# Optimization experiments

Measured on AMD Instinct MI355X. Metric: run time of the kernel, lower is better.

## Reference

```python
import jax, jax.numpy as jnp
import numpy as np

B, N, S, D, H = 32, 16384, 8, 64, 128  # batch, num_inputs, num_slots, slot_size(==input_size), mlp_hidden
ITERS = 3
EPS = 1e-8
LN_EPS = 1e-5


def _ln(x, g, b):
    m = jnp.mean(x, axis=-1, keepdims=True)
    v = jnp.mean((x - m) ** 2, axis=-1, keepdims=True)
    return (x - m) * jax.lax.rsqrt(v + LN_EPS) * g + b


def setup_inputs() -> dict:
    key = jax.random.key(0)
    ks = jax.random.split(key, 20)
    s = 0.02
    return {
        "x": jax.random.normal(ks[0], (B, N, D), jnp.float32),
        "slot_noise": jax.random.normal(ks[1], (B, S, D), jnp.float32),
        "slots_mu": jax.random.normal(ks[2], (1, S, D), jnp.float32),
        "slots_log_sigma": jax.random.normal(ks[3], (1, S, D), jnp.float32) * 0.1,
        "ln_in_g": jnp.ones((D,), jnp.float32), "ln_in_b": jnp.zeros((D,), jnp.float32),
        "ln_slot_g": jnp.ones((D,), jnp.float32), "ln_slot_b": jnp.zeros((D,), jnp.float32),
        "ln_mlp_g": jnp.ones((D,), jnp.float32), "ln_mlp_b": jnp.zeros((D,), jnp.float32),
        "Wq": jax.random.normal(ks[4], (D, D), jnp.float32) * s,
        "Wk": jax.random.normal(ks[5], (D, D), jnp.float32) * s,
        "Wv": jax.random.normal(ks[6], (D, D), jnp.float32) * s,
        "W_ih": jax.random.normal(ks[7], (3 * D, D), jnp.float32) * s,
        "W_hh": jax.random.normal(ks[8], (3 * D, D), jnp.float32) * s,
        "b_ih": jnp.zeros((3 * D,), jnp.float32),
        "b_hh": jnp.zeros((3 * D,), jnp.float32),
        "W1": jax.random.normal(ks[9], (H, D), jnp.float32) * s,
        "b1": jnp.zeros((H,), jnp.float32),
        "W2": jax.random.normal(ks[10], (D, H), jnp.float32) * s,
        "b2": jnp.zeros((D,), jnp.float32),
    }


def reference(x, slot_noise, slots_mu, slots_log_sigma,
              ln_in_g, ln_in_b, ln_slot_g, ln_slot_b, ln_mlp_g, ln_mlp_b,
              Wq, Wk, Wv, W_ih, W_hh, b_ih, b_hh, W1, b1, W2, b2):
    inputs = _ln(x, ln_in_g, ln_in_b)                      # [B,N,D]
    keys = inputs @ Wk.T                                   # [B,N,D]
    values = inputs @ Wv.T                                 # [B,N,D]
    slots = slots_mu + jnp.exp(slots_log_sigma) * slot_noise  # [B,S,D]
    scale = D ** (-0.5)
    for _ in range(ITERS):
        slots_prev = slots
        q = (_ln(slots, ln_slot_g, ln_slot_b) @ Wq.T) * scale   # [B,S,D]
        attn = jax.nn.softmax(jnp.einsum('bnd,bsd->bns', keys, q), axis=2) + EPS
        attn = attn / jnp.sum(attn, axis=1, keepdims=True)      # weighted mean over inputs
        updates = jnp.einsum('bns,bnd->bsd', attn, values)      # [B,S,D]
        # GRUCell(update, hidden=slots_prev), torch semantics
        gi = updates @ W_ih.T + b_ih
        gh = slots_prev @ W_hh.T + b_hh
        i_r, i_z, i_n = jnp.split(gi, 3, axis=-1)
        h_r, h_z, h_n = jnp.split(gh, 3, axis=-1)
        r = jax.nn.sigmoid(i_r + h_r)
        z = jax.nn.sigmoid(i_z + h_z)
        n = jnp.tanh(i_n + r * h_n)
        upd = (1.0 - z) * n + z * slots_prev
        # residual MLP (full_skip=False: residual around updates)
        slots = upd + jax.nn.relu(_ln(upd, ln_mlp_g, ln_mlp_b) @ W1.T + b1) @ W2.T + b2
    return slots
```

## Files before the change

kernel.cpp:

```cpp
#include <hip/hip_runtime.h>

#define BB 32
#define NN 16384

typedef __attribute__((ext_vector_type(4))) float f4;
typedef __attribute__((ext_vector_type(8))) short short8;

__device__ __forceinline__ unsigned int f2bf(float f) {
  unsigned int u = __float_as_uint(f);
  return (u + 0x7fffu + ((u >> 16) & 1u)) >> 16;
}
__device__ __forceinline__ short bfs(float f) { return (short)f2bf(f); }

__global__ void __launch_bounds__(256) prep_kernel(
    const float* __restrict__ Wk, const float* __restrict__ Wv,
    unsigned short* __restrict__ Wkb, unsigned short* __restrict__ Wvb)
{
  int id = blockIdx.x * 256 + threadIdx.x;
  Wkb[id] = (unsigned short)f2bf(Wk[id]);
  Wvb[id] = (unsigned short)f2bf(Wv[id]);
}

__global__ void __launch_bounds__(64) init_q_kernel(
    const float* __restrict__ noise, const float* __restrict__ mu,
    const float* __restrict__ lsig, float* __restrict__ slots,
    const float* __restrict__ gs, const float* __restrict__ bsl,
    const float* __restrict__ Wq, unsigned short* __restrict__ qb)
{
  const int bsi = blockIdx.x, l = threadIdx.x;
  const int idx = bsi * 64 + l;
  __shared__ float sh[64];
  float v = mu[idx & 511] + __expf(lsig[idx & 511]) * noise[idx];
  slots[idx] = v;
  float sm = v, sq = v * v;
#pragma unroll
  for (int m = 1; m < 64; m <<= 1) { sm += __shfl_xor(sm, m); sq += __shfl_xor(sq, m); }
  float mean = sm * (1.f / 64.f);
  float var = sq * (1.f / 64.f) - mean * mean;
  sh[l] = (v - mean) * rsqrtf(var + 1e-5f) * gs[l] + bsl[l];
  float acc = 0.f;
  const float* w = Wq + l * 64;
  for (int k = 0; k < 64; ++k) acc += sh[k] * w[k];
  qb[idx] = (unsigned short)f2bf(acc * 0.125f);
}

__global__ void __launch_bounds__(256) proj_kernel(
    const float* __restrict__ x, const float* __restrict__ gin, const float* __restrict__ bin,
    const unsigned short* __restrict__ Wkb, const unsigned short* __restrict__ Wvb,
    unsigned short* __restrict__ Kf, unsigned short* __restrict__ Vtf)
{
  const int blk = blockIdx.x;
  const int tid = threadIdx.x, wave = tid >> 6, lane = tid & 63;
  const int l15 = lane & 15, quad = lane >> 4;
  const int b = blk >> 6;
  const size_t row0 = ((size_t)blk << 8) + (wave << 4) + l15;
  const float* xp = x + row0 * 64 + quad * 8;

  const int k0 = quad * 8;
  f4 g0a = *(const f4*)(gin + k0),      g0b = *(const f4*)(gin + k0 + 4);
  f4 g1a = *(const f4*)(gin + k0 + 32), g1b = *(const f4*)(gin + k0 + 36);
  f4 h0a = *(const f4*)(bin + k0),      h0b = *(const f4*)(bin + k0 + 4);
  f4 h1a = *(const f4*)(bin + k0 + 32), h1b = *(const f4*)(bin + k0 + 36);

  f4 c0 = *(const f4*)xp, c1 = *(const f4*)(xp + 4);
  f4 c2 = *(const f4*)(xp + 32), c3 = *(const f4*)(xp + 36);

  for (int g = 0; g < 4; ++g) {
    f4 p0, p1, p2, p3;
    if (g < 3) {
      const float* np = xp + (size_t)(g + 1) * 4096;
      p0 = *(const f4*)np;        p1 = *(const f4*)(np + 4);
      p2 = *(const f4*)(np + 32); p3 = *(const f4*)(np + 36);
    }
    float sm = 0.f, sq = 0.f;
#pragma unroll
    for (int j = 0; j < 4; ++j) {
      float v0 = c0[j], v1 = c1[j], v2 = c2[j], v3 = c3[j];
      sm += v0 + v1 + v2 + v3;
      sq += v0 * v0 + v1 * v1 + v2 * v2 + v3 * v3;
    }
    sm += __shfl_xor(sm, 16); sq += __shfl_xor(sq, 16);
    sm += __shfl_xor(sm, 32); sq += __shfl_xor(sq, 32);
    const float mean = sm * (1.f / 64.f);
    const float var = sq * (1.f / 64.f) - mean * mean;
    const float rstd = rsqrtf(var + 1e-5f);

    short8 a0, a1;
#pragma unroll
    for (int j = 0; j < 4; ++j) {
      a0[j]     = bfs((c0[j] - mean) * rstd * g0a[j] + h0a[j]);
      a0[j + 4] = bfs((c1[j] - mean) * rstd * g0b[j] + h0b[j]);
      a1[j]     = bfs((c2[j] - mean) * rstd * g1a[j] + h1a[j]);
      a1[j + 4] = bfs((c3[j] - mean) * rstd * g1b[j] + h1b[j]);
    }

    const int nblk = ((blk & 63) << 4) + (g << 2) + wave;
    unsigned short* kbase = Kf + (((size_t)b << 20) + (nblk << 10));
    unsigned short* vbase = Vtf + (((size_t)b << 20) + (nblk << 10));

#pragma unroll
    for (int dt = 0; dt < 4; ++dt) {
      const unsigned short* wkp = Wkb + ((dt << 4) + l15) * 64 + k0;
      const unsigned short* wvp = Wvb + ((dt << 4) + l15) * 64 + k0;
      short8 wk0 = *(const short8*)wkp, wk1 = *(const short8*)(wkp + 32);
      short8 wv0 = *(const short8*)wvp, wv1 = *(const short8*)(wvp + 32);
      f4 ak = {0.f, 0.f, 0.f, 0.f}, av = {0.f, 0.f, 0.f, 0.f};
      ak = __builtin_amdgcn_mfma_f32_16x16x32_bf16(wk0, a0, ak, 0, 0, 0);
      ak = __builtin_amdgcn_mfma_f32_16x16x32_bf16(wk1, a1, ak, 0, 0, 0);
      av = __builtin_amdgcn_mfma_f32_16x16x32_bf16(a0, wv0, av, 0, 0, 0);
      av = __builtin_amdgcn_mfma_f32_16x16x32_bf16(a1, wv1, av, 0, 0, 0);
      uint2 kk;
      kk.x = f2bf(ak[0]) | (f2bf(ak[1]) << 16);
      kk.y = f2bf(ak[2]) | (f2bf(ak[3]) << 16);
      *(uint2*)(kbase + (((dt << 1) + (quad >> 1)) << 7) + (l15 << 3) + ((quad & 1) << 2)) = kk;
      uint2 vv;
      vv.x = f2bf(av[0]) | (f2bf(av[1]) << 16);
      vv.y = f2bf(av[2]) | (f2bf(av[3]) << 16);
      *(uint2*)(vbase + (((dt << 4) + l15) << 4) + (quad << 2)) = vv;
    }
    c0 = p0; c1 = p1; c2 = p2; c3 = p3;
  }
}

__global__ void __launch_bounds__(256) reduce_kernel(
    const unsigned short* __restrict__ Kf, const unsigned short* __restrict__ Vtf,
    const unsigned short* __restrict__ qb,
    float* __restrict__ Wpart, float* __restrict__ cpart)
{
  __shared__ __align__(16) unsigned short Pt[4][16][40];
  __shared__ float red[4][512];
  __shared__ float cred[4][8];

  const int tid = threadIdx.x, wave = tid >> 6, lane = tid & 63;
  const int l15 = lane & 15, quad = lane >> 4;
  const int b = blockIdx.x >> 6, ch = blockIdx.x & 63;

  const unsigned short* qrow = qb + (((b << 3) + (l15 & 7)) << 6) + quad * 8;
  short8 qf0 = *(const short8*)qrow;
  short8 qf1 = *(const short8*)(qrow + 32);

  const unsigned short* Kb = Kf + ((size_t)b << 20);
  const unsigned short* Vb = Vtf + ((size_t)b << 20);

  f4 wacc[4];
#pragma unroll
  for (int t = 0; t < 4; ++t) wacc[t] = (f4){0.f, 0.f, 0.f, 0.f};
  float cacc = 0.f;
  const int nb0 = (ch << 8) + (wave << 6);

#pragma unroll
  for (int u = 0; u < 2; ++u) {
    const int nb = nb0 + u * 32;
    const int nblk0 = nb >> 4;
    const unsigned short* ka = Kb + (nblk0 << 10) + (quad << 7) + (l15 << 3);
    short8 ka0 = *(const short8*)ka;
    short8 ka1 = *(const short8*)(ka + 512);
    short8 kb0 = *(const short8*)(ka + 1024);
    short8 kb1 = *(const short8*)(ka + 1536);
    short8 vf[4];
#pragma unroll
    for (int t = 0; t < 4; ++t)
      vf[t] = *(const short8*)(Vb + ((nblk0 + (quad >> 1)) << 10) +
                               (((t << 4) + l15) << 4) + ((quad & 1) << 3));

#pragma unroll
    for (int h = 0; h < 2; ++h) {
      f4 lg = {0.f, 0.f, 0.f, 0.f};
      lg = __builtin_amdgcn_mfma_f32_16x16x32_bf16(h ? kb0 : ka0, qf0, lg, 0, 0, 0);
      lg = __builtin_amdgcn_mfma_f32_16x16x32_bf16(h ? kb1 : ka1, qf1, lg, 0, 0, 0);
      float p[4];
#pragma unroll
      for (int r2 = 0; r2 < 4; ++r2) {
        float e = __expf(lg[r2]);
        float ss = e;
        ss += __shfl_xor(ss, 1);
        ss += __shfl_xor(ss, 2);
        ss += __shfl_xor(ss, 4);
        p[r2] = e * __builtin_amdgcn_rcpf(ss);
        cacc += p[r2];
      }
      unsigned short* pw = &Pt[wave][l15][h * 16 + quad * 4];
      *(unsigned int*)pw = f2bf(p[0]) | (f2bf(p[1]) << 16);
      *(unsigned int*)(pw + 2) = f2bf(p[2]) | (f2bf(p[3]) << 16);
    }
    short8 pf = *(const short8*)&Pt[wave][l15][quad * 8];
#pragma unroll
    for (int t = 0; t < 4; ++t)
      wacc[t] = __builtin_amdgcn_mfma_f32_16x16x32_bf16(pf, vf[t], wacc[t], 0, 0, 0);
  }

  cacc += __shfl_xor(cacc, 16);
  cacc += __shfl_xor(cacc, 32);
  if (lane < 8) cred[wave][lane] = cacc;
  if (quad < 2) {
#pragma unroll
    for (int t = 0; t < 4; ++t)
#pragma unroll
      for (int r2 = 0; r2 < 4; ++r2)
        red[wave][(quad * 4 + r2) * 64 + (t << 4) + l15] = wacc[t][r2];
  }
  __syncthreads();
  for (int i = tid; i < 512; i += 256)
    Wpart[(size_t)blockIdx.x * 512 + i] = red[0][i] + red[1][i] + red[2][i] + red[3][i];
  if (tid < 8)
    cpart[blockIdx.x * 8 + tid] = cred[0][tid] + cred[1][tid] + cred[2][tid] + cred[3][tid];
}

__global__ void __launch_bounds__(256) update_kernel(
    const float* __restrict__ Wpart, const float* __restrict__ cpart,
    const float* __restrict__ slots, float* __restrict__ out,
    const float* __restrict__ W_ih, const float* __restrict__ W_hh,
    const float* __restrict__ b_ih, const float* __restrict__ b_hh,
    const float* __restrict__ g_mlp, const float* __restrict__ b_mlp,
    const float* __restrict__ W1, const float* __restrict__ b1,
    const float* __restrict__ W2, const float* __restrict__ b2,
    const float* __restrict__ gs, const float* __restrict__ bsl,
    const float* __restrict__ Wq, unsigned short* __restrict__ qb, int make_q)
{
  const int bs = blockIdx.x;
  const int b = bs >> 3, s = bs & 7;
  const int tid = threadIdx.x;
  const int l = tid & 63, cq = tid >> 6;
  __shared__ float wred[4][64];
  __shared__ float credS[4];
  __shared__ float u_sh[64], sp_sh[64], giA[192], ghA[192], uln_sh[64], h_sh[128];

  float wp = 0.f, cp2 = 0.f;
  for (int c = cq * 16; c < cq * 16 + 16; ++c) {
    wp += Wpart[(size_t)(((b << 6) + c) * 8 + s) * 64 + l];
    cp2 += cpart[((b << 6) + c) * 8 + s];
  }
  wred[cq][l] = wp;
  if (l == 0) credS[cq] = cp2;
  __syncthreads();

  float sp = 0.f;
  if (tid < 64) {
    const float cs = credS[0] + credS[1] + credS[2] + credS[3];
    const float u = (wred[0][l] + wred[1][l] + wred[2][l] + wred[3][l]) / cs;
    sp = slots[(b * 8 + s) * 64 + l];
    u_sh[l] = u; sp_sh[l] = sp;
  }
  __syncthreads();

  if (tid < 192) {
    float accI = b_ih[tid], accH = b_hh[tid];
    const float* wi = W_ih + tid * 64;
    const float* wh = W_hh + tid * 64;
    for (int k = 0; k < 64; ++k) { accI += u_sh[k] * wi[k]; accH += sp_sh[k] * wh[k]; }
    giA[tid] = accI; ghA[tid] = accH;
  }
  __syncthreads();

  float upd = 0.f;
  if (tid < 64) {
    const float rg = 1.f / (1.f + __expf(-(giA[l] + ghA[l])));
    const float zg = 1.f / (1.f + __expf(-(giA[64 + l] + ghA[64 + l])));
    const float ng = tanhf(giA[128 + l] + rg * ghA[128 + l]);
    upd = (1.f - zg) * ng + zg * sp;
    float sm = upd, sq = upd * upd;
#pragma unroll
    for (int m = 1; m < 64; m <<= 1) { sm += __shfl_xor(sm, m); sq += __shfl_xor(sq, m); }
    const float mean = sm * (1.f / 64.f);
    const float var = sq * (1.f / 64.f) - mean * mean;
    uln_sh[l] = (upd - mean) * rsqrtf(var + 1e-5f) * g_mlp[l] + b_mlp[l];
  }
  __syncthreads();

  if (tid < 128) {
    float acc = b1[tid];
    const float* w1 = W1 + tid * 64;
    for (int k = 0; k < 64; ++k) acc += uln_sh[k] * w1[k];
    h_sh[tid] = fmaxf(acc, 0.f);
  }
  __syncthreads();

  if (tid < 64) {
    float acc = b2[l];
    const float* w2 = W2 + l * 128;
    for (int k = 0; k < 128; ++k) acc += h_sh[k] * w2[k];
    const float sv = upd + acc;
    out[(b * 8 + s) * 64 + l] = sv;
    if (make_q) {
      float sm2 = sv, sq2 = sv * sv;
#pragma unroll
      for (int m = 1; m < 64; m <<= 1) { sm2 += __shfl_xor(sm2, m); sq2 += __shfl_xor(sq2, m); }
      const float mean2 = sm2 * (1.f / 64.f);
      const float var2 = sq2 * (1.f / 64.f) - mean2 * mean2;
      u_sh[l] = (sv - mean2) * rsqrtf(var2 + 1e-5f) * gs[l] + bsl[l];
      float qa = 0.f;
      const float* w = Wq + l * 64;
      for (int k = 0; k < 64; ++k) qa += u_sh[k] * w[k];
      qb[(b * 8 + s) * 64 + l] = (unsigned short)f2bf(qa * 0.125f);
    }
  }
}

extern "C" void kernel_launch(void* const* d_in, const int* in_sizes, int n_in,
                              void* d_out, int out_size, void* d_ws, size_t ws_size,
                              hipStream_t stream) {
  const float* x       = (const float*)d_in[0];
  const float* noise   = (const float*)d_in[1];
  const float* mu      = (const float*)d_in[2];
  const float* lsig    = (const float*)d_in[3];
  const float* ln_in_g = (const float*)d_in[4];
  const float* ln_in_b = (const float*)d_in[5];
  const float* ln_sl_g = (const float*)d_in[6];
  const float* ln_sl_b = (const float*)d_in[7];
  const float* ln_ml_g = (const float*)d_in[8];
  const float* ln_ml_b = (const float*)d_in[9];
  const float* Wq      = (const float*)d_in[10];
  const float* Wk      = (const float*)d_in[11];
  const float* Wv      = (const float*)d_in[12];
  const float* W_ih    = (const float*)d_in[13];
  const float* W_hh    = (const float*)d_in[14];
  const float* b_ih    = (const float*)d_in[15];
  const float* b_hh    = (const float*)d_in[16];
  const float* W1      = (const float*)d_in[17];
  const float* b1      = (const float*)d_in[18];
  const float* W2      = (const float*)d_in[19];
  const float* b2      = (const float*)d_in[20];

  unsigned short* Kw  = (unsigned short*)d_ws;
  unsigned short* Vt  = Kw + (size_t)BB * NN * 64;
  unsigned short* Wkb = Vt + (size_t)BB * NN * 64;
  unsigned short* Wvb = Wkb + 4096;
  unsigned short* qb  = Wvb + 4096;
  float* slots = (float*)(qb + 16384);
  float* Wpart = slots + 32 * 8 * 64;
  float* cpart = Wpart + (size_t)2048 * 512;

  prep_kernel<<<dim3(16), dim3(256), 0, stream>>>(Wk, Wv, Wkb, Wvb);
  init_q_kernel<<<dim3(256), dim3(64), 0, stream>>>(
      noise, mu, lsig, slots, ln_sl_g, ln_sl_b, Wq, qb);
  proj_kernel<<<dim3(2048), dim3(256), 0, stream>>>(
      x, ln_in_g, ln_in_b, Wkb, Wvb, Kw, Vt);

  for (int it = 0; it < 3; ++it) {
    reduce_kernel<<<dim3(2048), dim3(256), 0, stream>>>(Kw, Vt, qb, Wpart, cpart);
    update_kernel<<<dim3(256), dim3(256), 0, stream>>>(
        Wpart, cpart, slots, (it == 2) ? (float*)d_out : slots,
        W_ih, W_hh, b_ih, b_hh, ln_ml_g, ln_ml_b, W1, b1, W2, b2,
        ln_sl_g, ln_sl_b, Wq, qb, (it < 2) ? 1 : 0);
  }
}
```

Measured before the change: 350.7 us.

## Restructure K layout and softmax mapping; hoist x loads and reuse weight fragments

The projection kernel now loads and normalizes all four row groups first, then loops over output tiles with each weight fragment reused across the four groups. K is written in a new interleaved layout. In the reduce kernel the MFMA operand order is swapped so slots land on rows, which shortens the softmax reduction to one cross-lane shuffle. Probabilities are written transposed into LDS as single 16-bit stores. The column-sum accumulation now reads the bf16-rounded probabilities from LDS, which changes rounding slightly. Scalar LDS stores may cause bank conflicts, and holding more live registers may lower occupancy.

```diff
diff --git a/kernel.cpp b/kernel.cpp
--- a/kernel.cpp
+++ b/kernel.cpp
@@ -11,6 +11,9 @@
   return (u + 0x7fffu + ((u >> 16) & 1u)) >> 16;
 }
 __device__ __forceinline__ short bfs(float f) { return (short)f2bf(f); }
+__device__ __forceinline__ float bf2f(unsigned short h) {
+  return __uint_as_float(((unsigned int)h) << 16);
+}
 
 __global__ void __launch_bounds__(256) prep_kernel(
     const float* __restrict__ Wk, const float* __restrict__ Wv,
@@ -47,7 +50,7 @@
 __global__ void __launch_bounds__(256) proj_kernel(
     const float* __restrict__ x, const float* __restrict__ gin, const float* __restrict__ bin,
     const unsigned short* __restrict__ Wkb, const unsigned short* __restrict__ Wvb,
-    unsigned short* __restrict__ Kf, unsigned short* __restrict__ Vtf)
+    unsigned short* __restrict__ Ktb, unsigned short* __restrict__ Vtf)
 {
   const int blk = blockIdx.x;
   const int tid = threadIdx.x, wave = tid >> 6, lane = tid & 63;
@@ -55,75 +58,73 @@
   const int b = blk >> 6;
   const size_t row0 = ((size_t)blk << 8) + (wave << 4) + l15;
   const float* xp = x + row0 * 64 + quad * 8;
-
   const int k0 = quad * 8;
+
   f4 g0a = *(const f4*)(gin + k0),      g0b = *(const f4*)(gin + k0 + 4);
   f4 g1a = *(const f4*)(gin + k0 + 32), g1b = *(const f4*)(gin + k0 + 36);
   f4 h0a = *(const f4*)(bin + k0),      h0b = *(const f4*)(bin + k0 + 4);
   f4 h1a = *(const f4*)(bin + k0 + 32), h1b = *(const f4*)(bin + k0 + 36);
 
-  f4 c0 = *(const f4*)xp, c1 = *(const f4*)(xp + 4);
-  f4 c2 = *(const f4*)(xp + 32), c3 = *(const f4*)(xp + 36);
-
+  short8 a0[4], a1[4];
+#pragma unroll
   for (int g = 0; g < 4; ++g) {
-    f4 p0, p1, p2, p3;
-    if (g < 3) {
-      const float* np = xp + (size_t)(g + 1) * 4096;
-      p0 = *(const f4*)np;        p1 = *(const f4*)(np + 4);
-      p2 = *(const f4*)(np + 32); p3 = *(const f4*)(np + 36);
-    }
+    const float* p = xp + (size_t)g * 4096;
+    f4 c0 = *(const f4*)p,        c1 = *(const f4*)(p + 4);
+    f4 c2 = *(const f4*)(p + 32), c3 = *(const f4*)(p + 36);
     float sm = 0.f, sq = 0.f;
 #pragma unroll
     for (int j = 0; j < 4; ++j) {
-      float v0 = c0[j], v1 = c1[j], v2 = c2[j], v3 = c3[j];
-      sm += v0 + v1 + v2 + v3;
-      sq += v0 * v0 + v1 * v1 + v2 * v2 + v3 * v3;
+      sm += c0[j] + c1[j] + c2[j] + c3[j];
+      sq += c0[j]*c0[j] + c1[j]*c1[j] + c2[j]*c2[j] + c3[j]*c3[j];
     }
     sm += __shfl_xor(sm, 16); sq += __shfl_xor(sq, 16);
     sm += __shfl_xor(sm, 32); sq += __shfl_xor(sq, 32);
     const float mean = sm * (1.f / 64.f);
     const float var = sq * (1.f / 64.f) - mean * mean;
     const float rstd = rsqrtf(var + 1e-5f);
-
-    short8 a0, a1;
 #pragma unroll
     for (int j = 0; j < 4; ++j) {
-      a0[j]     = bfs((c0[j] - mean) * rstd * g0a[j] + h0a[j]);
-      a0[j + 4] = bfs((c1[j] - mean) * rstd * g0b[j] + h0b[j]);
-      a1[j]     = bfs((c2[j] - mean) * rstd * g1a[j] + h1a[j]);
-      a1[j + 4] = bfs((c3[j] - mean) * rstd * g1b[j] + h1b[j]);
-    }
-
-    const int nblk = ((blk & 63) << 4) + (g << 2) + wave;
-    unsigned short* kbase = Kf + (((size_t)b << 20) + (nblk << 10));
-    unsigned short* vbase = Vtf + (((size_t)b << 20) + (nblk << 10));
-
-#pragma unroll
-    for (int dt = 0; dt < 4; ++dt) {
-      const unsigned short* wkp = Wkb + ((dt << 4) + l15) * 64 + k0;
-      const unsigned short* wvp = Wvb + ((dt << 4) + l15) * 64 + k0;
-      short8 wk0 = *(const short8*)wkp, wk1 = *(const short8*)(wkp + 32);
-      short8 wv0 = *(const short8*)wvp, wv1 = *(const short8*)(wvp + 32);
+      a0[g][j]     = bfs((c0[j] - mean) * rstd * g0a[j] + h0a[j]);
+      a0[g][j + 4] = bfs((c1[j] - mean) * rstd * g0b[j] + h0b[j]);
+      a1[g][j]     = bfs((c2[j] - mean) * rstd * g1a[j] + h1a[j]);
+      a1[g][j + 4] = bfs((c3[j] - mean) * rstd * g1b[j] + h1b[j]);
+    }
+  }
+
+  const int nblk0 = ((blk & 63) << 4) + wave;
+  unsigned short* Kbase = Ktb + ((size_t)b << 20);
+  unsigned short* Vbase = Vtf + ((size_t)b << 20);
+
+#pragma unroll
+  for (int dt = 0; dt < 4; ++dt) {
+    const unsigned short* wkp = Wkb + ((dt << 4) + l15) * 64 + k0;
+    const unsigned short* wvp = Wvb + ((dt << 4) + l15) * 64 + k0;
+    short8 wk0 = *(const short8*)wkp, wk1 = *(const short8*)(wkp + 32);
+    short8 wv0 = *(const short8*)wvp, wv1 = *(const short8*)(wvp + 32);
+    const int koff = ((dt >> 1) << 9) + (l15 << 5) +
+                     ((((dt & 1) << 1) | (quad >> 1)) << 3) + ((quad & 1) << 2);
+    const int voff = (((dt << 4) + l15) << 4) + (quad << 2);
+#pragma unroll
+    for (int g = 0; g < 4; ++g) {
       f4 ak = {0.f, 0.f, 0.f, 0.f}, av = {0.f, 0.f, 0.f, 0.f};
-      ak = __builtin_amdgcn_mfma_f32_16x16x32_bf16(wk0, a0, ak, 0, 0, 0);
-      ak = __builtin_amdgcn_mfma_f32_16x16x32_bf16(wk1, a1, ak, 0, 0, 0);
-      av = __builtin_amdgcn_mfma_f32_16x16x32_bf16(a0, wv0, av, 0, 0, 0);
-      av = __builtin_amdgcn_mfma_f32_16x16x32_bf16(a1, wv1, av, 0, 0, 0);
-      uint2 kk;
+      ak = __builtin_amdgcn_mfma_f32_16x16x32_bf16(wk0, a0[g], ak, 0, 0, 0);
+      ak = __builtin_amdgcn_mfma_f32_16x16x32_bf16(wk1, a1[g], ak, 0, 0, 0);
+      av = __builtin_amdgcn_mfma_f32_16x16x32_bf16(a0[g], wv0, av, 0, 0, 0);
+      av = __builtin_amdgcn_mfma_f32_16x16x32_bf16(a1[g], wv1, av, 0, 0, 0);
+      const size_t nb10 = (size_t)(nblk0 + (g << 2)) << 10;
+      uint2 kk, vv;
       kk.x = f2bf(ak[0]) | (f2bf(ak[1]) << 16);
       kk.y = f2bf(ak[2]) | (f2bf(ak[3]) << 16);
-      *(uint2*)(kbase + (((dt << 1) + (quad >> 1)) << 7) + (l15 << 3) + ((quad & 1) << 2)) = kk;
-      uint2 vv;
       vv.x = f2bf(av[0]) | (f2bf(av[1]) << 16);
       vv.y = f2bf(av[2]) | (f2bf(av[3]) << 16);
-      *(uint2*)(vbase + (((dt << 4) + l15) << 4) + (quad << 2)) = vv;
-    }
-    c0 = p0; c1 = p1; c2 = p2; c3 = p3;
+      *(uint2*)(Kbase + nb10 + koff) = kk;
+      *(uint2*)(Vbase + nb10 + voff) = vv;
+    }
   }
 }
 
 __global__ void __launch_bounds__(256) reduce_kernel(
-    const unsigned short* __restrict__ Kf, const unsigned short* __restrict__ Vtf,
+    const unsigned short* __restrict__ Ktb, const unsigned short* __restrict__ Vtf,
     const unsigned short* __restrict__ qb,
     float* __restrict__ Wpart, float* __restrict__ cpart)
 {
@@ -139,7 +140,7 @@
   short8 qf0 = *(const short8*)qrow;
   short8 qf1 = *(const short8*)(qrow + 32);
 
-  const unsigned short* Kb = Kf + ((size_t)b << 20);
+  const unsigned short* Kb = Ktb + ((size_t)b << 20);
   const unsigned short* Vb = Vtf + ((size_t)b << 20);
 
   f4 wacc[4];
@@ -150,40 +151,37 @@
 
 #pragma unroll
   for (int u = 0; u < 2; ++u) {
-    const int nb = nb0 + u * 32;
-    const int nblk0 = nb >> 4;
-    const unsigned short* ka = Kb + (nblk0 << 10) + (quad << 7) + (l15 << 3);
-    short8 ka0 = *(const short8*)ka;
-    short8 ka1 = *(const short8*)(ka + 512);
-    short8 kb0 = *(const short8*)(ka + 1024);
-    short8 kb1 = *(const short8*)(ka + 1536);
+    const int nblk0 = (nb0 + u * 32) >> 4;
+    const unsigned short* kp = Kb + (nblk0 << 10) + (l15 << 5) + (quad << 3);
+    short8 k00 = *(const short8*)kp;
+    short8 k01 = *(const short8*)(kp + 512);
+    short8 k10 = *(const short8*)(kp + 1024);
+    short8 k11 = *(const short8*)(kp + 1536);
     short8 vf[4];
 #pragma unroll
     for (int t = 0; t < 4; ++t)
-      vf[t] = *(const short8*)(Vb + ((nblk0 + (quad >> 1)) << 10) +
+      vf[t] = *(const short8*)(Vb + ((size_t)(nblk0 + (quad >> 1)) << 10) +
                                (((t << 4) + l15) << 4) + ((quad & 1) << 3));
 
 #pragma unroll
-    for (int h = 0; h < 2; ++h) {
+    for (int nt = 0; nt < 2; ++nt) {
       f4 lg = {0.f, 0.f, 0.f, 0.f};
-      lg = __builtin_amdgcn_mfma_f32_16x16x32_bf16(h ? kb0 : ka0, qf0, lg, 0, 0, 0);
-      lg = __builtin_amdgcn_mfma_f32_16x16x32_bf16(h ? kb1 : ka1, qf1, lg, 0, 0, 0);
-      float p[4];
-#pragma unroll
-      for (int r2 = 0; r2 < 4; ++r2) {
-        float e = __expf(lg[r2]);
-        float ss = e;
-        ss += __shfl_xor(ss, 1);
-        ss += __shfl_xor(ss, 2);
-        ss += __shfl_xor(ss, 4);
-        p[r2] = e * __builtin_amdgcn_rcpf(ss);
-        cacc += p[r2];
-      }
-      unsigned short* pw = &Pt[wave][l15][h * 16 + quad * 4];
-      *(unsigned int*)pw = f2bf(p[0]) | (f2bf(p[1]) << 16);
-      *(unsigned int*)(pw + 2) = f2bf(p[2]) | (f2bf(p[3]) << 16);
+      lg = __builtin_amdgcn_mfma_f32_16x16x32_bf16(qf0, nt ? k10 : k00, lg, 0, 0, 0);
+      lg = __builtin_amdgcn_mfma_f32_16x16x32_bf16(qf1, nt ? k11 : k01, lg, 0, 0, 0);
+      float e0 = __expf(lg[0]), e1 = __expf(lg[1]);
+      float e2 = __expf(lg[2]), e3 = __expf(lg[3]);
+      float ss = (e0 + e1) + (e2 + e3);
+      ss += __shfl_xor(ss, 16);
+      const float inv = __builtin_amdgcn_rcpf(ss);
+      const int col = nt * 16 + l15;
+      Pt[wave][quad * 4 + 0][col] = (unsigned short)f2bf(e0 * inv);
+      Pt[wave][quad * 4 + 1][col] = (unsigned short)f2bf(e1 * inv);
+      Pt[wave][quad * 4 + 2][col] = (unsigned short)f2bf(e2 * inv);
+      Pt[wave][quad * 4 + 3][col] = (unsigned short)f2bf(e3 * inv);
     }
     short8 pf = *(const short8*)&Pt[wave][l15][quad * 8];
+#pragma unroll
+    for (int i = 0; i < 8; ++i) cacc += bf2f((unsigned short)pf[i]);
 #pragma unroll
     for (int t = 0; t < 4; ++t)
       wacc[t] = __builtin_amdgcn_mfma_f32_16x16x32_bf16(pf, vf[t], wacc[t], 0, 0, 0);
@@ -321,8 +319,8 @@
   const float* W2      = (const float*)d_in[19];
   const float* b2      = (const float*)d_in[20];
 
-  unsigned short* Kw  = (unsigned short*)d_ws;
-  unsigned short* Vt  = Kw + (size_t)BB * NN * 64;
+  unsigned short* Ktb = (unsigned short*)d_ws;
+  unsigned short* Vt  = Ktb + (size_t)BB * NN * 64;
   unsigned short* Wkb = Vt + (size_t)BB * NN * 64;
   unsigned short* Wvb = Wkb + 4096;
   unsigned short* qb  = Wvb + 4096;
@@ -334,10 +332,10 @@
   init_q_kernel<<<dim3(256), dim3(64), 0, stream>>>(
       noise, mu, lsig, slots, ln_sl_g, ln_sl_b, Wq, qb);
   proj_kernel<<<dim3(2048), dim3(256), 0, stream>>>(
-      x, ln_in_g, ln_in_b, Wkb, Wvb, Kw, Vt);
+      x, ln_in_g, ln_in_b, Wkb, Wvb, Ktb, Vt);
 
   for (int it = 0; it < 3; ++it) {
-    reduce_kernel<<<dim3(2048), dim3(256), 0, stream>>>(Kw, Vt, qb, Wpart, cpart);
+    reduce_kernel<<<dim3(2048), dim3(256), 0, stream>>>(Ktb, Vt, qb, Wpart, cpart);
     update_kernel<<<dim3(256), dim3(256), 0, stream>>>(
         Wpart, cpart, slots, (it == 2) ? (float*)d_out : slots,
         W_ih, W_hh, b_ih, b_hh, ln_ml_g, ln_ml_b, W1, b1, W2, b2,
```

After: 361.7 us. +3.1%, slower.

## Halve proj/reduce grids and software-pipeline K/V loads in reduce kernel

Applied to the files above, without the earlier changes.

Proj and reduce kernels now each handle 512 rows per block instead of 256, so each grid shrinks from 2048 to 1024 blocks. The reduce kernel gains a register double-buffered loop that prefetches the next 32-row K/V tile while the current tile's logits, softmax and value accumulation run. This aims to hide global load latency and cut the partial-sum traffic and work in the update kernel. The cost is more registers per thread and fewer blocks to spread across the GPU's compute units.

```diff
diff --git a/kernel.cpp b/kernel.cpp
--- a/kernel.cpp
+++ b/kernel.cpp
@@ -52,8 +52,8 @@
   const int blk = blockIdx.x;
   const int tid = threadIdx.x, wave = tid >> 6, lane = tid & 63;
   const int l15 = lane & 15, quad = lane >> 4;
-  const int b = blk >> 6;
-  const size_t row0 = ((size_t)blk << 8) + (wave << 4) + l15;
+  const int b = blk >> 5;
+  const size_t row0 = ((size_t)blk << 9) + (wave << 4) + l15;
   const float* xp = x + row0 * 64 + quad * 8;
 
   const int k0 = quad * 8;
@@ -65,9 +65,9 @@
   f4 c0 = *(const f4*)xp, c1 = *(const f4*)(xp + 4);
   f4 c2 = *(const f4*)(xp + 32), c3 = *(const f4*)(xp + 36);
 
-  for (int g = 0; g < 4; ++g) {
+  for (int g = 0; g < 8; ++g) {
     f4 p0, p1, p2, p3;
-    if (g < 3) {
+    if (g < 7) {
       const float* np = xp + (size_t)(g + 1) * 4096;
       p0 = *(const f4*)np;        p1 = *(const f4*)(np + 4);
       p2 = *(const f4*)(np + 32); p3 = *(const f4*)(np + 36);
@@ -94,7 +94,7 @@
       a1[j + 4] = bfs((c3[j] - mean) * rstd * g1b[j] + h1b[j]);
     }
 
-    const int nblk = ((blk & 63) << 4) + (g << 2) + wave;
+    const int nblk = ((blk & 31) << 5) + (g << 2) + wave;
     unsigned short* kbase = Kf + (((size_t)b << 20) + (nblk << 10));
     unsigned short* vbase = Vtf + (((size_t)b << 20) + (nblk << 10));
 
@@ -133,7 +133,7 @@
 
   const int tid = threadIdx.x, wave = tid >> 6, lane = tid & 63;
   const int l15 = lane & 15, quad = lane >> 4;
-  const int b = blockIdx.x >> 6, ch = blockIdx.x & 63;
+  const int b = blockIdx.x >> 5, ch = blockIdx.x & 31;
 
   const unsigned short* qrow = qb + (((b << 3) + (l15 & 7)) << 6) + quad * 8;
   short8 qf0 = *(const short8*)qrow;
@@ -146,28 +146,42 @@
 #pragma unroll
   for (int t = 0; t < 4; ++t) wacc[t] = (f4){0.f, 0.f, 0.f, 0.f};
   float cacc = 0.f;
-  const int nb0 = (ch << 8) + (wave << 6);
-
-#pragma unroll
-  for (int u = 0; u < 2; ++u) {
-    const int nb = nb0 + u * 32;
-    const int nblk0 = nb >> 4;
-    const unsigned short* ka = Kb + (nblk0 << 10) + (quad << 7) + (l15 << 3);
-    short8 ka0 = *(const short8*)ka;
-    short8 ka1 = *(const short8*)(ka + 512);
-    short8 kb0 = *(const short8*)(ka + 1024);
-    short8 kb1 = *(const short8*)(ka + 1536);
-    short8 vf[4];
+  const int nblk_base = (ch << 5) + (wave << 3);
+
+  short8 ck[4], cv[4];
+  {
+    const unsigned short* ka = Kb + (nblk_base << 10) + (quad << 7) + (l15 << 3);
+    ck[0] = *(const short8*)ka;
+    ck[1] = *(const short8*)(ka + 512);
+    ck[2] = *(const short8*)(ka + 1024);
+    ck[3] = *(const short8*)(ka + 1536);
 #pragma unroll
     for (int t = 0; t < 4; ++t)
-      vf[t] = *(const short8*)(Vb + ((nblk0 + (quad >> 1)) << 10) +
+      cv[t] = *(const short8*)(Vb + ((size_t)(nblk_base + (quad >> 1)) << 10) +
                                (((t << 4) + l15) << 4) + ((quad & 1) << 3));
+  }
+
+#pragma unroll
+  for (int u = 0; u < 4; ++u) {
+    short8 nk[4], nv[4];
+    if (u < 3) {
+      const int nblk = nblk_base + 2 * (u + 1);
+      const unsigned short* ka = Kb + (nblk << 10) + (quad << 7) + (l15 << 3);
+      nk[0] = *(const short8*)ka;
+      nk[1] = *(const short8*)(ka + 512);
+      nk[2] = *(const short8*)(ka + 1024);
+      nk[3] = *(const short8*)(ka + 1536);
+#pragma unroll
+      for (int t = 0; t < 4; ++t)
+        nv[t] = *(const short8*)(Vb + ((size_t)(nblk + (quad >> 1)) << 10) +
+                                 (((t << 4) + l15) << 4) + ((quad & 1) << 3));
+    }
 
 #pragma unroll
     for (int h = 0; h < 2; ++h) {
       f4 lg = {0.f, 0.f, 0.f, 0.f};
-      lg = __builtin_amdgcn_mfma_f32_16x16x32_bf16(h ? kb0 : ka0, qf0, lg, 0, 0, 0);
-      lg = __builtin_amdgcn_mfma_f32_16x16x32_bf16(h ? kb1 : ka1, qf1, lg, 0, 0, 0);
+      lg = __builtin_amdgcn_mfma_f32_16x16x32_bf16(ck[h * 2], qf0, lg, 0, 0, 0);
+      lg = __builtin_amdgcn_mfma_f32_16x16x32_bf16(ck[h * 2 + 1], qf1, lg, 0, 0, 0);
       float p[4];
 #pragma unroll
       for (int r2 = 0; r2 < 4; ++r2) {
@@ -186,7 +200,10 @@
     short8 pf = *(const short8*)&Pt[wave][l15][quad * 8];
 #pragma unroll
     for (int t = 0; t < 4; ++t)
-      wacc[t] = __builtin_amdgcn_mfma_f32_16x16x32_bf16(pf, vf[t], wacc[t], 0, 0, 0);
+      wacc[t] = __builtin_amdgcn_mfma_f32_16x16x32_bf16(pf, cv[t], wacc[t], 0, 0, 0);
+
+#pragma unroll
+    for (int i = 0; i < 4; ++i) { ck[i] = nk[i]; cv[i] = nv[i]; }
   }
 
   cacc += __shfl_xor(cacc, 16);
@@ -226,9 +243,9 @@
   __shared__ float u_sh[64], sp_sh[64], giA[192], ghA[192], uln_sh[64], h_sh[128];
 
   float wp = 0.f, cp2 = 0.f;
-  for (int c = cq * 16; c < cq * 16 + 16; ++c) {
-    wp += Wpart[(size_t)(((b << 6) + c) * 8 + s) * 64 + l];
-    cp2 += cpart[((b << 6) + c) * 8 + s];
+  for (int c = cq * 8; c < cq * 8 + 8; ++c) {
+    wp += Wpart[(size_t)(((b << 5) + c) * 8 + s) * 64 + l];
+    cp2 += cpart[((b << 5) + c) * 8 + s];
   }
   wred[cq][l] = wp;
   if (l == 0) credS[cq] = cp2;
@@ -328,16 +345,16 @@
   unsigned short* qb  = Wvb + 4096;
   float* slots = (float*)(qb + 16384);
   float* Wpart = slots + 32 * 8 * 64;
-  float* cpart = Wpart + (size_t)2048 * 512;
+  float* cpart = Wpart + (size_t)1024 * 512;
 
   prep_kernel<<<dim3(16), dim3(256), 0, stream>>>(Wk, Wv, Wkb, Wvb);
   init_q_kernel<<<dim3(256), dim3(64), 0, stream>>>(
       noise, mu, lsig, slots, ln_sl_g, ln_sl_b, Wq, qb);
-  proj_kernel<<<dim3(2048), dim3(256), 0, stream>>>(
+  proj_kernel<<<dim3(1024), dim3(256), 0, stream>>>(
       x, ln_in_g, ln_in_b, Wkb, Wvb, Kw, Vt);
 
   for (int it = 0; it < 3; ++it) {
-    reduce_kernel<<<dim3(2048), dim3(256), 0, stream>>>(Kw, Vt, qb, Wpart, cpart);
+    reduce_kernel<<<dim3(1024), dim3(256), 0, stream>>>(Kw, Vt, qb, Wpart, cpart);
     update_kernel<<<dim3(256), dim3(256), 0, stream>>>(
         Wpart, cpart, slots, (it == 2) ? (float*)d_out : slots,
         W_ih, W_hh, b_ih, b_hh, ln_ml_g, ln_ml_b, W1, b1, W2, b2,
```

Measured after the change: 345.1 us. About the same (-1.6%).
